# Kernel tuning notes

Hardware: AMD Instinct MI355X
Metric: run time of the kernel (lower is better)

Reference implementation:

```python
import jax, jax.numpy as jnp
import numpy as np

N = 50000
E = 800000
F_IN = 128
HID = 64
OUT = 64
H = 4
NEG_SLOPE = 0.2


def setup_inputs() -> dict:
    key = jax.random.key(0)
    ks = jax.random.split(key, 10)
    s = lambda fan_in: 1.0 / np.sqrt(fan_in)
    x = jax.random.normal(ks[0], (N, F_IN), dtype=jnp.float32)
    edge_index = jax.random.randint(ks[1], (2, E), 0, N, dtype=jnp.int64)
    # layer 1: in -> hid, heads H, concat=False
    W1 = jax.random.normal(ks[2], (F_IN, H * HID), dtype=jnp.float32) * s(F_IN)
    a_src1 = jax.random.normal(ks[3], (H, HID), dtype=jnp.float32) * s(HID)
    a_dst1 = jax.random.normal(ks[4], (H, HID), dtype=jnp.float32) * s(HID)
    b1 = jnp.zeros((HID,), dtype=jnp.float32)
    # layer 2: hid -> out
    W2 = jax.random.normal(ks[5], (HID, H * OUT), dtype=jnp.float32) * s(HID)
    a_src2 = jax.random.normal(ks[6], (H, OUT), dtype=jnp.float32) * s(OUT)
    a_dst2 = jax.random.normal(ks[7], (H, OUT), dtype=jnp.float32) * s(OUT)
    b2 = jnp.zeros((OUT,), dtype=jnp.float32)
    return {"x": x, "edge_index": edge_index, "W1": W1, "a_src1": a_src1,
            "a_dst1": a_dst1, "b1": b1, "W2": W2, "a_src2": a_src2,
            "a_dst2": a_dst2, "b2": b2}


def gat_layer(x, src, dst, W, a_s, a_d, b):
    n, h, c = x.shape[0], a_s.shape[0], a_s.shape[1]
    hfeat = (x @ W).reshape(n, h, c)                      # [N,H,C]
    # per-node attention halves, gathered per edge
    alpha_src = jnp.einsum('nhc,hc->nh', hfeat, a_s)       # [N,H]
    alpha_dst = jnp.einsum('nhc,hc->nh', hfeat, a_d)
    e = alpha_src[src] + alpha_dst[dst]                    # [E,H]
    e = jnp.where(e >= 0, e, NEG_SLOPE * e)                # LeakyReLU(0.2)
    # segment softmax over destination node neighborhoods
    m = jax.ops.segment_max(e, dst, num_segments=n)
    e = jnp.exp(e - m[dst])
    denom = jax.ops.segment_sum(e, dst, num_segments=n)
    alpha = e / (denom[dst] + 1e-16)                       # [E,H]
    msg = hfeat[src] * alpha[:, :, None]                   # [E,H,C]
    out = jax.ops.segment_sum(msg, dst, num_segments=n)    # [N,H,C]
    return out.mean(axis=1) + b                            # concat=False -> head mean


def reference(x, edge_index, W1, a_src1, a_dst1, b1, W2, a_src2, a_dst2, b2):
    src, dst = edge_index[0], edge_index[1]
    h = gat_layer(x, src, dst, W1, a_src1, a_dst1, b1)
    h = jax.nn.relu(h)
    h = gat_layer(h, src, dst, W2, a_src2, a_dst2, b2)
    return jax.nn.log_softmax(h, axis=1)
```

## Files before the change

kernel.cpp:

```cpp
#include <hip/hip_runtime.h>
#include <math.h>

constexpr int NNODE = 50000;
constexpr int FIN   = 128;
constexpr int HID   = 64;
constexpr int NH    = 4;
constexpr int NC    = 256;
constexpr float NEG = 0.2f;
constexpr int MPAD  = 50048;
constexpr int SCANB = (NNODE + 255) / 256;

typedef unsigned short u16;
typedef unsigned int   u32;
typedef __fp16 h16x8 __attribute__((ext_vector_type(8)));
typedef __fp16 h2    __attribute__((ext_vector_type(2)));
typedef float  f32x4 __attribute__((ext_vector_type(4)));

__device__ __forceinline__ u16 f2h(float f) {
  union { __fp16 h; u16 u; } c; c.h = (__fp16)f; return c.u;
}
__device__ __forceinline__ h2 u2h2(u32 u) {
  union { u32 u; h2 h; } c; c.u = u; return c.h;
}
__device__ __forceinline__ float readlane_f(float v, int l) {
  return __int_as_float(__builtin_amdgcn_readlane(__float_as_int(v), l));
}
__device__ __forceinline__ u32 h2bf8(u16 hx) {
  return ((u32)hx + 0x7Fu + ((hx >> 8) & 1u)) >> 8;
}

__global__ __launch_bounds__(256) void count_pack(const int* __restrict__ ei, int* __restrict__ deg,
                                                  int* __restrict__ rank, int E, int edgeBlocks,
                                                  const float* __restrict__ W1, const float* __restrict__ W2,
                                                  u16* __restrict__ Bp1, u16* __restrict__ Bp2) {
  int b = blockIdx.x;
  if (b < edgeBlocks) {
    int i = b * 256 + threadIdx.x;
    if (i < E) rank[i] = atomicAdd(&deg[ei[E + i]], 1);
  } else {
    int i = (b - edgeBlocks) * 256 + threadIdx.x;
    const int t1 = FIN * NC;
    const int t2 = HID * NC;
    if (i < t1) {
      int k = i >> 8, c = i & 255;
      Bp1[((size_t)(k >> 3) * 256 + c) * 8 + (k & 7)] = f2h(W1[i]);
    } else if (i < t1 + t2) {
      int j = i - t1;
      int k = j >> 8, c = j & 255;
      Bp2[((size_t)(k >> 3) * 256 + c) * 8 + (k & 7)] = f2h(W2[j]);
    }
  }
}

__global__ __launch_bounds__(256) void scan_phase1(const int* __restrict__ deg,
                                                   int* __restrict__ blockSums, int n) {
  __shared__ int sm[256];
  int tid = threadIdx.x;
  int i = blockIdx.x * 256 + tid;
  sm[tid] = (i < n) ? deg[i] : 0;
  __syncthreads();
#pragma unroll
  for (int o = 128; o > 0; o >>= 1) {
    if (tid < o) sm[tid] += sm[tid + o];
    __syncthreads();
  }
  if (tid == 0) blockSums[blockIdx.x] = sm[0];
}

__global__ __launch_bounds__(256) void scan_phase23(const int* __restrict__ blockSums,
                                                    const int* __restrict__ deg,
                                                    int* __restrict__ offs, int n) {
  __shared__ int ss[256];
  __shared__ int sm[256];
  int tid = threadIdx.x;
  ss[tid] = (tid < SCANB) ? blockSums[tid] : 0;
  __syncthreads();
#pragma unroll
  for (int o = 1; o < 256; o <<= 1) {
    int t = (tid >= o) ? ss[tid - o] : 0;
    __syncthreads();
    ss[tid] += t;
    __syncthreads();
  }
  int blockOff = (blockIdx.x == 0) ? 0 : ss[blockIdx.x - 1];
  int i = blockIdx.x * 256 + tid;
  int v = (i < n) ? deg[i] : 0;
  sm[tid] = v;
  __syncthreads();
#pragma unroll
  for (int o = 1; o < 256; o <<= 1) {
    int t = (tid >= o) ? sm[tid - o] : 0;
    __syncthreads();
    sm[tid] += t;
    __syncthreads();
  }
  int ex = sm[tid] - v + blockOff;
  if (i < n) offs[i] = ex;
  if (blockIdx.x == SCANB - 1 && tid == 255) offs[n] = ss[SCANB - 1];
}

template <int KS, bool AF32, bool F8>
__device__ __forceinline__ void gemm_body(
    int bx, const void* __restrict__ Aptr, const u16* __restrict__ Bp,
    const float* __restrict__ a_s, const float* __restrict__ a_d,
    void* __restrict__ feat, float* __restrict__ al_s, float* __restrict__ al_d, int M) {
  const int K = 32 * KS;
  int lane = threadIdx.x & 63;
  int wv = threadIdx.x >> 6;
  int q = lane >> 4, r = lane & 15;
  int m0 = bx * 64 + wv * 16;

  h16x8 af[KS];
  if (AF32) {
    int ar = m0 + r; if (ar >= M) ar = M - 1;
    const float* arow = (const float*)Aptr + (size_t)ar * K + q * 8;
#pragma unroll
    for (int ks = 0; ks < KS; ++ks) {
      float4 v0 = *(const float4*)(arow + ks * 32);
      float4 v1 = *(const float4*)(arow + ks * 32 + 4);
      union { h16x8 v; h2 p[4]; } u;
      u.p[0] = __builtin_amdgcn_cvt_pkrtz(v0.x, v0.y);
      u.p[1] = __builtin_amdgcn_cvt_pkrtz(v0.z, v0.w);
      u.p[2] = __builtin_amdgcn_cvt_pkrtz(v1.x, v1.y);
      u.p[3] = __builtin_amdgcn_cvt_pkrtz(v1.z, v1.w);
      af[ks] = u.v;
    }
  } else {
    const u16* arow = (const u16*)Aptr + (size_t)(m0 + r) * K + q * 8;
#pragma unroll
    for (int ks = 0; ks < KS; ++ks) af[ks] = *(const h16x8*)(arow + ks * 32);
  }

  int node_base = m0 + q * 4;
  u32 pk8[4][4];
  if (F8) {
#pragma unroll
    for (int a = 0; a < 4; ++a)
#pragma unroll
      for (int b = 0; b < 4; ++b) pk8[a][b] = 0u;
  }
#pragma unroll
  for (int h = 0; h < NH; ++h) {
    f32x4 acc[4];
#pragma unroll
    for (int c4 = 0; c4 < 4; ++c4) {
      acc[c4] = (f32x4){0.f, 0.f, 0.f, 0.f};
      const u16* bp = Bp + ((size_t)q * 256 + (h * 4 + c4) * 16 + r) * 8;
#pragma unroll
      for (int ks = 0; ks < KS; ++ks) {
        h16x8 bf = *(const h16x8*)(bp + (size_t)ks * 4 * 256 * 8);
        acc[c4] = __builtin_amdgcn_mfma_f32_16x16x32_f16(af[ks], bf, acc[c4], 0, 0, 0);
      }
    }
    float ps[4] = {0.f, 0.f, 0.f, 0.f}, pd[4] = {0.f, 0.f, 0.f, 0.f};
#pragma unroll
    for (int c4 = 0; c4 < 4; ++c4) {
      float sa = a_s[h * HID + c4 * 16 + r];
      float da = a_d[h * HID + c4 * 16 + r];
#pragma unroll
      for (int reg = 0; reg < 4; ++reg) {
        float v = acc[c4][reg];
        ps[reg] += v * sa;
        pd[reg] += v * da;
        if (F8) {
          pk8[c4][reg] |= h2bf8(f2h(v)) << (8 * h);
        } else {
          int node = node_base + reg;
          if (node < M) ((u16*)feat)[(size_t)node * NC + (c4 * 16 + r) * NH + h] = f2h(v);
        }
      }
    }
#pragma unroll
    for (int reg = 0; reg < 4; ++reg) {
#pragma unroll
      for (int o = 1; o < 16; o <<= 1) {
        ps[reg] += __shfl_xor(ps[reg], o);
        pd[reg] += __shfl_xor(pd[reg], o);
      }
      int node = node_base + reg;
      if (r == 0 && node < M) {
        al_s[node * NH + h] = ps[reg];
        al_d[node * NH + h] = pd[reg];
      }
    }
  }
  if (F8) {
#pragma unroll
    for (int c4 = 0; c4 < 4; ++c4)
#pragma unroll
      for (int reg = 0; reg < 4; ++reg) {
        int node = node_base + reg;
        if (node < M)
          *(u32*)((char*)feat + (size_t)node * 256 + (c4 * 16 + r) * 4) = pk8[c4][reg];
      }
  }
}

__global__ __launch_bounds__(256) void gemm1_scatter(
    const float* __restrict__ x, const u16* __restrict__ Bp1,
    const float* __restrict__ a_s, const float* __restrict__ a_d,
    void* __restrict__ hf8, float* __restrict__ al_s, float* __restrict__ al_d, int M,
    const int* __restrict__ ei, const int* __restrict__ offs, const int* __restrict__ rank,
    int* __restrict__ csr_src, int E, int gemmBlocks) {
  int b = blockIdx.x;
  if (b < gemmBlocks) {
    gemm_body<4, true, true>(b, x, Bp1, a_s, a_d, hf8, al_s, al_d, M);
  } else {
    int i = (b - gemmBlocks) * 256 + threadIdx.x;
    if (i < E) {
      int dst = ei[E + i];
      csr_src[offs[dst] + rank[i]] = ei[i];
    }
  }
}

__global__ __launch_bounds__(256) void gemm2_kernel(
    const u16* __restrict__ h1bf, const u16* __restrict__ Bp2,
    const float* __restrict__ a_s, const float* __restrict__ a_d,
    void* __restrict__ hf8, float* __restrict__ al_s, float* __restrict__ al_d, int M) {
  gemm_body<2, false, true>(blockIdx.x, h1bf, Bp2, a_s, a_d, hf8, al_s, al_d, M);
}

template <bool FINAL, bool F8>
__global__ __launch_bounds__(256) void agg_kernel(const void* __restrict__ feat,
                                                  const float4* __restrict__ al_s4,
                                                  const float4* __restrict__ al_d4,
                                                  const int* __restrict__ offs,
                                                  const int* __restrict__ csr,
                                                  const float* __restrict__ bias,
                                                  void* __restrict__ out_v, int n) {
  int lane = threadIdx.x & 63;
  int node = blockIdx.x * 4 + (threadIdx.x >> 6);
  if (node >= n) return;
  float4 ad = al_d4[node];
  int lj = lane & 7;
  int hsel = (lane >> 3) & 3;
  float adv = hsel == 0 ? ad.x : (hsel == 1 ? ad.y : (hsel == 2 ? ad.z : ad.w));
  h2 acc01 = {(__fp16)0.f, (__fp16)0.f};
  h2 acc23 = {(__fp16)0.f, (__fp16)0.f};
  float dacc = 0.f;
  int s = offs[node], e = offs[node + 1];
  int nch = (e - s + 7) >> 3;
  int i = s;
  int voff = F8 ? lane * 4 : lane * 8;

  int vidx = 0;
  float4 as = make_float4(0.f, 0.f, 0.f, 0.f);
  uint2 hv[8];
  if (nch > 0) {
    int id0 = i + lj; if (id0 >= e) id0 = e - 1;
    vidx = csr[id0];
    as = al_s4[vidx];
#pragma unroll
    for (int j = 0; j < 8; ++j) {
      int sa = __builtin_amdgcn_readlane(vidx, j);
      if (F8) hv[j].x = *(const u32*)((const char*)feat + (size_t)sa * 256 + voff);
      else    hv[j]   = *(const uint2*)((const char*)feat + (size_t)sa * 512 + voff);
    }
  }

  for (int ch = 0; ch < nch; ++ch) {
    bool last = (ch + 1 == nch);
    float asv = hsel == 0 ? as.x : (hsel == 1 ? as.y : (hsel == 2 ? as.z : as.w));
    float ev = asv + adv;
    ev = ev >= 0.f ? ev : NEG * ev;
    float wv = __expf(ev - 1.3862944f);
    if (i + lj >= e) wv = 0.f;
    float t = wv;
    t += __shfl_xor(t, 1); t += __shfl_xor(t, 2); t += __shfl_xor(t, 4);
    dacc += t;
    float w8 = __shfl_xor(wv, 8);
    union { h2 h; u32 u; } pc;
    pc.h = __builtin_amdgcn_cvt_pkrtz(wv, w8);
    int vidx_n = 0;
    float4 as_n = make_float4(0.f, 0.f, 0.f, 0.f);
    uint2 hn[8];
    if (!last) {
      int id1 = i + 8 + lj; if (id1 >= e) id1 = e - 1;
      vidx_n = csr[id1];
      as_n = al_s4[vidx_n];
#pragma unroll
      for (int j = 0; j < 8; ++j) {
        int sa = __builtin_amdgcn_readlane(vidx_n, j);
        if (F8) hn[j].x = *(const u32*)((const char*)feat + (size_t)sa * 256 + voff);
        else    hn[j]   = *(const uint2*)((const char*)feat + (size_t)sa * 512 + voff);
      }
    }
#pragma unroll
    for (int j = 0; j < 8; ++j) {
      u32 w01 = (u32)__builtin_amdgcn_readlane((int)pc.u, j);
      u32 w23 = (u32)__builtin_amdgcn_readlane((int)pc.u, 16 + j);
      u32 f01, f23;
      if (F8) {
        f01 = __builtin_amdgcn_perm(0u, hv[j].x, 0x01080008u);
        f23 = __builtin_amdgcn_perm(0u, hv[j].x, 0x03080208u);
      } else {
        f01 = hv[j].x; f23 = hv[j].y;
      }
      acc01 += u2h2(w01) * u2h2(f01);
      acc23 += u2h2(w23) * u2h2(f23);
    }
    if (!last) {
      vidx = vidx_n; as = as_n;
#pragma unroll
      for (int j = 0; j < 8; ++j) hv[j] = hn[j];
    }
    i += 8;
  }
  float d0 = readlane_f(dacc, 0), d1 = readlane_f(dacc, 8);
  float d2 = readlane_f(dacc, 16), d3 = readlane_f(dacc, 24);
  float val = 0.25f * ((float)acc01.x / (d0 + 1e-16f) + (float)acc01.y / (d1 + 1e-16f) +
                       (float)acc23.x / (d2 + 1e-16f) + (float)acc23.y / (d3 + 1e-16f)) +
              bias[lane];
  if (!FINAL) {
    ((u16*)out_v)[(size_t)node * HID + lane] = f2h(fmaxf(val, 0.f));
  } else {
    float mx = val;
#pragma unroll
    for (int o = 32; o >= 1; o >>= 1) mx = fmaxf(mx, __shfl_xor(mx, o));
    float ex = __expf(val - mx);
    float sm = ex;
#pragma unroll
    for (int o = 32; o >= 1; o >>= 1) sm += __shfl_xor(sm, o);
    ((float*)out_v)[(size_t)node * HID + lane] = (val - mx) - logf(sm);
  }
}

extern "C" void kernel_launch(void* const* d_in, const int* in_sizes, int n_in,
                              void* d_out, int out_size, void* d_ws, size_t ws_size,
                              hipStream_t stream) {
  const float* x   = (const float*)d_in[0];
  const int*   ei  = (const int*)d_in[1];
  const float* W1  = (const float*)d_in[2];
  const float* as1 = (const float*)d_in[3];
  const float* ad1 = (const float*)d_in[4];
  const float* b1  = (const float*)d_in[5];
  const float* W2  = (const float*)d_in[6];
  const float* as2 = (const float*)d_in[7];
  const float* ad2 = (const float*)d_in[8];
  const float* b2  = (const float*)d_in[9];
  float* out = (float*)d_out;

  const int N = NNODE;
  const int E = in_sizes[1] / 2;

  char* base = (char*)d_ws;
  size_t off = 0;
  auto alloc = [&](size_t bytes) -> void* {
    void* p = base + off;
    off += (bytes + 255) & ~(size_t)255;
    return p;
  };
  u32*    hf8    = (u32*)alloc((size_t)N * 256);
  u16*    h1bf   = (u16*)alloc((size_t)MPAD * HID * 2);
  u16*    Bp1    = (u16*)alloc((size_t)FIN * NC * 2);
  u16*    Bp2    = (u16*)alloc((size_t)HID * NC * 2);
  float*  al_s   = (float*)alloc((size_t)N * NH * 4);
  float*  al_d   = (float*)alloc((size_t)N * NH * 4);
  int*    deg    = (int*)alloc((size_t)N * 4);
  int*    offs   = (int*)alloc((size_t)(N + 1) * 4);
  int*    rank   = (int*)alloc((size_t)E * 4);
  int*    csr    = (int*)alloc((size_t)(E + 16) * 4);
  int*    bsums  = (int*)alloc(256 * 4);

  const int edgeBlocks = (E + 255) / 256;
  const int gemmBlocks = MPAD / 64;
  const int nodeBlocks = (N + 3) / 4;
  const int packBlocks = (FIN * NC + HID * NC + 255) / 256;

  (void)hipMemsetAsync(deg, 0, (size_t)N * 4, stream);
  count_pack<<<edgeBlocks + packBlocks, 256, 0, stream>>>(ei, deg, rank, E, edgeBlocks, W1, W2, Bp1, Bp2);
  scan_phase1<<<SCANB, 256, 0, stream>>>(deg, bsums, N);
  scan_phase23<<<SCANB, 256, 0, stream>>>(bsums, deg, offs, N);

  gemm1_scatter<<<gemmBlocks + edgeBlocks, 256, 0, stream>>>(
      x, Bp1, as1, ad1, hf8, al_s, al_d, N,
      ei, offs, rank, csr, E, gemmBlocks);
  agg_kernel<false, true><<<nodeBlocks, 256, 0, stream>>>(hf8, (const float4*)al_s, (const float4*)al_d,
                                                          offs, csr, b1, h1bf, N);

  gemm2_kernel<<<gemmBlocks, 256, 0, stream>>>(h1bf, Bp2, as2, ad2, hf8, al_s, al_d, N);
  agg_kernel<true, true><<<nodeBlocks, 256, 0, stream>>>(hf8, (const float4*)al_s, (const float4*)al_d,
                                                         offs, csr, b2, out, N);
}
```

Baseline: 245.0 us.

## Fuse degree zeroing into weight pack and overlap edge counting with GEMM1

The memset of the degree array is replaced by zeroing blocks inside the weight-packing kernel. The atomic degree count is moved into the same launch as the first GEMM so the two run concurrently. The CSR scatter becomes its own kernel after the scan. Launch count stays the same, but the GEMM now shares its launch with atomics instead of with the scatter, and the scatter runs alone on the critical path.

```diff
diff --git a/kernel.cpp b/kernel.cpp
--- a/kernel.cpp
+++ b/kernel.cpp
@@ -29,16 +29,13 @@
   return ((u32)hx + 0x7Fu + ((hx >> 8) & 1u)) >> 8;
 }
 
-__global__ __launch_bounds__(256) void count_pack(const int* __restrict__ ei, int* __restrict__ deg,
-                                                  int* __restrict__ rank, int E, int edgeBlocks,
-                                                  const float* __restrict__ W1, const float* __restrict__ W2,
-                                                  u16* __restrict__ Bp1, u16* __restrict__ Bp2) {
+__global__ __launch_bounds__(256) void pack_zero(const float* __restrict__ W1,
+                                                 const float* __restrict__ W2,
+                                                 u16* __restrict__ Bp1, u16* __restrict__ Bp2,
+                                                 int* __restrict__ deg, int packBlocks, int n) {
   int b = blockIdx.x;
-  if (b < edgeBlocks) {
+  if (b < packBlocks) {
     int i = b * 256 + threadIdx.x;
-    if (i < E) rank[i] = atomicAdd(&deg[ei[E + i]], 1);
-  } else {
-    int i = (b - edgeBlocks) * 256 + threadIdx.x;
     const int t1 = FIN * NC;
     const int t2 = HID * NC;
     if (i < t1) {
@@ -49,6 +46,9 @@
       int k = j >> 8, c = j & 255;
       Bp2[((size_t)(k >> 3) * 256 + c) * 8 + (k & 7)] = f2h(W2[j]);
     }
+  } else {
+    int i = (b - packBlocks) * 256 + threadIdx.x;
+    if (i < n) deg[i] = 0;
   }
 }
 
@@ -196,21 +196,28 @@
   }
 }
 
-__global__ __launch_bounds__(256) void gemm1_scatter(
+__global__ __launch_bounds__(256) void count_gemm1(
     const float* __restrict__ x, const u16* __restrict__ Bp1,
     const float* __restrict__ a_s, const float* __restrict__ a_d,
     void* __restrict__ hf8, float* __restrict__ al_s, float* __restrict__ al_d, int M,
-    const int* __restrict__ ei, const int* __restrict__ offs, const int* __restrict__ rank,
-    int* __restrict__ csr_src, int E, int gemmBlocks) {
+    const int* __restrict__ ei, int* __restrict__ deg, int* __restrict__ rank,
+    int E, int gemmBlocks) {
   int b = blockIdx.x;
   if (b < gemmBlocks) {
     gemm_body<4, true, true>(b, x, Bp1, a_s, a_d, hf8, al_s, al_d, M);
   } else {
     int i = (b - gemmBlocks) * 256 + threadIdx.x;
-    if (i < E) {
-      int dst = ei[E + i];
-      csr_src[offs[dst] + rank[i]] = ei[i];
-    }
+    if (i < E) rank[i] = atomicAdd(&deg[ei[E + i]], 1);
+  }
+}
+
+__global__ __launch_bounds__(256) void scatter_kernel(
+    const int* __restrict__ ei, const int* __restrict__ offs,
+    const int* __restrict__ rank, int* __restrict__ csr_src, int E) {
+  int i = blockIdx.x * 256 + threadIdx.x;
+  if (i < E) {
+    int dst = ei[E + i];
+    csr_src[offs[dst] + rank[i]] = ei[i];
   }
 }
 
@@ -368,14 +375,16 @@
   const int nodeBlocks = (N + 3) / 4;
   const int packBlocks = (FIN * NC + HID * NC + 255) / 256;
 
-  (void)hipMemsetAsync(deg, 0, (size_t)N * 4, stream);
-  count_pack<<<edgeBlocks + packBlocks, 256, 0, stream>>>(ei, deg, rank, E, edgeBlocks, W1, W2, Bp1, Bp2);
+  pack_zero<<<packBlocks + SCANB, 256, 0, stream>>>(W1, W2, Bp1, Bp2, deg, packBlocks, N);
+
+  count_gemm1<<<gemmBlocks + edgeBlocks, 256, 0, stream>>>(
+      x, Bp1, as1, ad1, hf8, al_s, al_d, N,
+      ei, deg, rank, E, gemmBlocks);
+
   scan_phase1<<<SCANB, 256, 0, stream>>>(deg, bsums, N);
   scan_phase23<<<SCANB, 256, 0, stream>>>(bsums, deg, offs, N);
-
-  gemm1_scatter<<<gemmBlocks + edgeBlocks, 256, 0, stream>>>(
-      x, Bp1, as1, ad1, hf8, al_s, al_d, N,
-      ei, offs, rank, csr, E, gemmBlocks);
+  scatter_kernel<<<edgeBlocks, 256, 0, stream>>>(ei, offs, rank, csr, E);
+
   agg_kernel<false, true><<<nodeBlocks, 256, 0, stream>>>(hf8, (const float4*)al_s, (const float4*)al_d,
                                                           offs, csr, b1, h1bf, N);
 
```

Measured after the change: 248.1 us. About the same (+1.3%).
